# Kernel optimization log

Hardware: AMD Instinct MI355X
Metric: run time of the kernel (lower is better)

Reference implementation:

```python
import jax, jax.numpy as jnp
import numpy as np

B, N, CIN, COUT, K, L, NNZ = 4, 4096, 128, 128, 10, 50, 65536


def _spmm(idx, vals, X):
    # COO spmm: out[r] += vals * X[c]; idx: [2, nnz], X: [N, F]
    rows, cols = idx[0], idx[1]
    return jax.ops.segment_sum(vals[:, None] * X[cols], rows, num_segments=N)

_bspmm = jax.vmap(_spmm, in_axes=(0, 0, 0))  # batched over leading dim


def _hgnn_layer(phi_idx, phi_val, inv_idx, inv_val, fea, W, d):
    # original: ((phi @ diag(d)) @ phi_inv) @ (fea @ W)
    # identical math, evaluated right-to-left to stay sparse-dense only
    filt = jnp.einsum('bnc,co->bno', fea, W)            # [B,N,COUT]
    y = _bspmm(inv_idx, inv_val, filt)                  # phi_inv @ X
    y = d[None, :, None] * y                            # diag(d) @ .
    return _bspmm(phi_idx, phi_val, y)                  # phi @ .


def setup_inputs() -> dict:
    key = jax.random.key(0)
    ks = jax.random.split(key, 20)

    def coo(ki, kv):
        idx = jax.random.randint(ki, (B, 2, NNZ), 0, N, dtype=jnp.int32)
        val = jax.random.normal(kv, (B, NNZ), jnp.float32) * 0.05
        return idx, val

    phi1_idx, phi1_val = coo(ks[0], ks[1])
    phi1_inv_idx, phi1_inv_val = coo(ks[2], ks[3])
    phi2_idx, phi2_val = coo(ks[4], ks[5])
    phi2_inv_idx, phi2_inv_val = coo(ks[6], ks[7])
    fea = jax.random.normal(ks[8], (B, N, CIN), jnp.float32)
    joblst = jax.random.randint(ks[9], (B, L), 0, N, dtype=jnp.int64)

    xavier = float(np.sqrt(6.0 / (CIN + COUT)))
    W1 = jax.random.uniform(ks[10], (CIN, COUT), jnp.float32, -xavier, xavier)
    W2 = jax.random.uniform(ks[11], (CIN, COUT), jnp.float32, -xavier, xavier)
    d1 = jax.random.uniform(ks[12], (N,), jnp.float32, 0.9, 1.1)
    d2 = jax.random.uniform(ks[13], (N,), jnp.float32, 0.9, 1.1)
    s = float(1.0 / np.sqrt(N))
    W_ih = jax.random.uniform(ks[14], (N, COUT), jnp.float32, -s, s)
    W_hh = jax.random.uniform(ks[15], (N, N), jnp.float32, -s, s)
    b_ih = jax.random.uniform(ks[16], (N,), jnp.float32, -s, s)
    b_hh = jnp.zeros((N,), jnp.float32)
    sd = float(1.0 / np.sqrt(COUT))
    dense_W = jax.random.uniform(ks[17], (K, COUT), jnp.float32, -sd, sd)
    dense_b = jnp.zeros((K,), jnp.float32)
    item_emb = jax.random.normal(ks[18], (N, COUT), jnp.float32) * 0.01

    return dict(phi1_idx=phi1_idx, phi1_val=phi1_val, phi1_inv_idx=phi1_inv_idx,
                phi1_inv_val=phi1_inv_val, phi2_idx=phi2_idx, phi2_val=phi2_val,
                phi2_inv_idx=phi2_inv_idx, phi2_inv_val=phi2_inv_val,
                fea=fea, joblst=joblst, W1=W1, d1=d1, W2=W2, d2=d2,
                W_ih=W_ih, W_hh=W_hh, b_ih=b_ih, b_hh=b_hh,
                dense_W=dense_W, dense_b=dense_b, item_emb=item_emb)


def reference(phi1_idx, phi1_val, phi1_inv_idx, phi1_inv_val,
              phi2_idx, phi2_val, phi2_inv_idx, phi2_inv_val,
              fea, joblst, W1, d1, W2, d2, W_ih, W_hh, b_ih, b_hh,
              dense_W, dense_b, item_emb):
    # two hypergraph conv layers, summed
    out1 = _hgnn_layer(phi1_idx, phi1_val, phi1_inv_idx, phi1_inv_val, fea, W1, d1)
    out2 = _hgnn_layer(phi2_idx, phi2_val, phi2_inv_idx, phi2_inv_val, fea, W2, d2)
    res = out1 + out2                                   # [B,N,COUT]

    # RNN over job history embeddings (all joblst entries valid -> no -1 filter)
    xs = jnp.swapaxes(item_emb[joblst], 0, 1)           # [L,B,COUT]
    h0 = jnp.zeros((fea.shape[0], N), fea.dtype)

    def step(h, x):
        h = jnp.tanh(x @ W_ih.T + h @ W_hh.T + b_ih + b_hh)
        return h, None

    Emb, _ = jax.lax.scan(step, h0, xs)                 # last hidden: [B,N]

    res2 = jax.nn.gelu(jnp.einsum('bno,ko->bnk', res, dense_W) + dense_b,
                       approximate=False)               # [B,N,K]
    # (res3 * Emb2).permute back == res2 * gelu(Emb) broadcast over K
    return jax.nn.sigmoid(res2 * jax.nn.gelu(Emb, approximate=False)[:, :, None])
```

## Files before the change

kernel.cpp:

```cpp
#include <hip/hip_runtime.h>
#include <cstdint>
#include <cstddef>

#define NN   4096
#define LLC  50

__device__ __forceinline__ float bf2f(unsigned short u) {
    return __uint_as_float(((unsigned)u) << 16);
}
__device__ __forceinline__ unsigned short f2bf(float x) {
    unsigned b = __float_as_uint(x);
    return (unsigned short)((b + 0x7fffu + ((b >> 16) & 1u)) >> 16);
}

#if __has_builtin(__builtin_amdgcn_sdot4)
#define SDOT4(a, b, c) __builtin_amdgcn_sdot4((int)(a), (int)(b), (c), false)
#else
__device__ __forceinline__ int sdot4_sw(unsigned a, unsigned b, int c) {
    c += (int)(signed char)(a) * (int)(signed char)(b);
    c += (int)(signed char)(a >> 8) * (int)(signed char)(b >> 8);
    c += (int)(signed char)(a >> 16) * (int)(signed char)(b >> 16);
    c += (int)(signed char)(a >> 24) * (int)(signed char)(b >> 24);
    return c;
}
#define SDOT4(a, b, c) sdot4_sw((a), (b), (c))
#endif

#define DPPADD(v, ctrl, rmask) \
    ((v) + __builtin_amdgcn_update_dpp(0, (v), (ctrl), (rmask), 0xf, true))
__device__ __forceinline__ int wred64(int v) {
    v = DPPADD(v, 0x111, 0xf);
    v = DPPADD(v, 0x112, 0xf);
    v = DPPADD(v, 0x114, 0xf);
    v = DPPADD(v, 0x118, 0xf);
    v = DPPADD(v, 0x142, 0xa);
    v = DPPADD(v, 0x143, 0xc);
    return v;
}

__global__ __launch_bounds__(256) void k_w8(const float* __restrict__ W,
                                            uint4* __restrict__ out) {
    unsigned T = blockIdx.x * 256 + threadIdx.x;
    unsigned row = T >> 8, rem = T & 255;
    unsigned k4 = rem >> 6, lane = rem & 63;
    unsigned k0 = lane * 16 + k4 * 4;
    const float* src = W + ((size_t)row * 1024 + k0) * 4;
    unsigned q[4];
#pragma unroll
    for (int i = 0; i < 4; ++i) {
        float4 w = *(const float4*)(src + i * 4);
        int q0 = (int)rintf(fminf(fmaxf(w.x * 8192.f, -127.f), 127.f));
        int q1 = (int)rintf(fminf(fmaxf(w.y * 8192.f, -127.f), 127.f));
        int q2 = (int)rintf(fminf(fmaxf(w.z * 8192.f, -127.f), 127.f));
        int q3 = (int)rintf(fminf(fmaxf(w.w * 8192.f, -127.f), 127.f));
        q[i] = (q0 & 0xff) | ((q1 & 0xff) << 8) | ((q2 & 0xff) << 16) | ((q3 & 0xff) << 24);
    }
    out[(size_t)row * 256 + k4 * 64 + lane] = make_uint4(q[0], q[1], q[2], q[3]);
}

__global__ __launch_bounds__(128) void k_filt(const float* __restrict__ fea,
                                              const float* __restrict__ W1,
                                              const float* __restrict__ W2,
                                              unsigned short* __restrict__ f1,
                                              unsigned short* __restrict__ f2) {
    __shared__ float sfea[16][128];
    int t = threadIdx.x;
    int rb = blockIdx.x * 16;
    for (int r = 0; r < 16; ++r) sfea[r][t] = fea[(size_t)(rb + r) * 128 + t];
    __syncthreads();
    float a1[16], a2[16];
#pragma unroll
    for (int r = 0; r < 16; ++r) { a1[r] = 0.f; a2[r] = 0.f; }
    for (int c = 0; c < 128; c += 4) {
        float w10 = W1[(c + 0) * 128 + t], w11 = W1[(c + 1) * 128 + t];
        float w12 = W1[(c + 2) * 128 + t], w13 = W1[(c + 3) * 128 + t];
        float w20 = W2[(c + 0) * 128 + t], w21 = W2[(c + 1) * 128 + t];
        float w22 = W2[(c + 2) * 128 + t], w23 = W2[(c + 3) * 128 + t];
#pragma unroll
        for (int r = 0; r < 16; ++r) {
            float4 f = *(const float4*)&sfea[r][c];
            a1[r] += f.x * w10 + f.y * w11 + f.z * w12 + f.w * w13;
            a2[r] += f.x * w20 + f.y * w21 + f.z * w22 + f.w * w23;
        }
    }
#pragma unroll
    for (int r = 0; r < 16; ++r) {
        f1[(size_t)(rb + r) * 128 + t] = f2bf(a1[r]);
        f2[(size_t)(rb + r) * 128 + t] = f2bf(a2[r]);
    }
}

__global__ __launch_bounds__(256) void k_hist(const int* __restrict__ i0, const int* __restrict__ i1,
                                              const int* __restrict__ i2, const int* __restrict__ i3,
                                              int* __restrict__ counts) {
    __shared__ int lc[4096];
    int t = threadIdx.x;
#pragma unroll
    for (int i = 0; i < 16; ++i) lc[t + i * 256] = 0;
    __syncthreads();
    unsigned blk = blockIdx.x;
    unsigned s = blk >> 4, ch = blk & 15;
    unsigned m = s >> 2, b = s & 3;
    const int* ip = (m == 0) ? i0 : (m == 1) ? i1 : (m == 2) ? i2 : i3;
    unsigned base = b * 131072u + ch * 4096u;
#pragma unroll
    for (int i = 0; i < 16; ++i) {
        int r = ip[base + t + i * 256];
        atomicAdd(&lc[r], 1);
    }
    __syncthreads();
    int* cs = counts + s * 4096;
#pragma unroll
    for (int i = 0; i < 16; ++i) {
        int v = lc[t + i * 256];
        if (v) atomicAdd(cs + t + i * 256, v);
    }
}

__global__ __launch_bounds__(256) void k_scan(const int* __restrict__ counts,
                                              int* __restrict__ rowptr,
                                              int* __restrict__ cursor) {
    int s = blockIdx.x, t = threadIdx.x;
    int loc[16];
    int base = t * 16;
    const int* cs = counts + s * 4096;
    int run = 0;
#pragma unroll
    for (int i = 0; i < 16; ++i) { loc[i] = run; run += cs[base + i]; }
    int total = run;
    int lane = t & 63, wv = t >> 6;
    int v = total;
#pragma unroll
    for (int d = 1; d < 64; d <<= 1) { int u = __shfl_up(v, d, 64); if (lane >= d) v += u; }
    __shared__ int wt[4];
    if (lane == 63) wt[wv] = v;
    __syncthreads();
    int pre = v - total;
    for (int i = 0; i < wv; ++i) pre += wt[i];
    int* rp = rowptr + s * 4097;
    int* cu = cursor + s * 4096;
#pragma unroll
    for (int i = 0; i < 16; ++i) { rp[base + i] = pre + loc[i]; cu[base + i] = pre + loc[i]; }
    if (t == 255) rp[4096] = pre + total;
}

__global__ __launch_bounds__(256) void k_scatter(const int* __restrict__ i0, const int* __restrict__ i1,
                                                 const int* __restrict__ i2, const int* __restrict__ i3,
                                                 const float* __restrict__ v0, const float* __restrict__ v1,
                                                 const float* __restrict__ v2, const float* __restrict__ v3,
                                                 const float* __restrict__ d1, const float* __restrict__ d2,
                                                 int* __restrict__ cursor,
                                                 unsigned* __restrict__ ep) {
    unsigned gid = blockIdx.x * 256 + threadIdx.x;
    unsigned s = gid >> 16, e = gid & 65535;
    unsigned m = s >> 2, b = s & 3;
    const int* ip = (m == 0) ? i0 : (m == 1) ? i1 : (m == 2) ? i2 : i3;
    const float* vp = (m == 0) ? v0 : (m == 1) ? v1 : (m == 2) ? v2 : v3;
    int r = ip[(size_t)b * 131072 + e];
    int c = ip[(size_t)b * 131072 + 65536 + e];
    float v = vp[(size_t)b * 65536 + e];
    if (m == 1) v *= d1[c];
    if (m == 3) v *= d2[c];
    int pos = atomicAdd(cursor + s * 4096 + r, 1);
    ep[(size_t)s * 65536 + pos] = ((unsigned)c << 16) | (unsigned)f2bf(v);
}

__global__ __launch_bounds__(128) void k_gather1(const int* __restrict__ rowptr,
                                                 const unsigned* __restrict__ ep,
                                                 const unsigned short* __restrict__ filt1,
                                                 const unsigned short* __restrict__ filt2,
                                                 unsigned short* __restrict__ y1,
                                                 unsigned short* __restrict__ y2) {
    unsigned blk = blockIdx.x;
    unsigned b = blk & 3, row = (blk >> 2) & 4095, mm = blk >> 14;
    int s = (mm ? 8 : 0) + (int)b;
    const unsigned short* X = mm ? filt2 : filt1;
    unsigned short* Y = mm ? y2 : y1;
    int f = threadIdx.x;
    const int* rp = rowptr + s * 4097;
    int e0 = rp[row], e1 = rp[row + 1];
    float acc = 0.f;
    for (int e = e0; e < e1; ++e) {
        unsigned p = ep[(size_t)s * 65536 + e];
        float v = bf2f((unsigned short)(p & 0xffffu));
        int c = (int)(p >> 16);
        acc += v * bf2f(X[((size_t)b * 4096 + c) * 128 + f]);
    }
    Y[((size_t)b * 4096 + row) * 128 + f] = f2bf(acc);
}

__global__ __launch_bounds__(128) void k_gather2(const int* __restrict__ rowptr,
                                                 const unsigned* __restrict__ ep,
                                                 const unsigned short* __restrict__ y1,
                                                 const unsigned short* __restrict__ y2,
                                                 float* __restrict__ res) {
    unsigned blk = blockIdx.x;
    unsigned b = blk & 3, row = blk >> 2;
    int f = threadIdx.x;
    float acc = 0.f;
    {
        int s = 4 + (int)b;
        const int* rp = rowptr + s * 4097;
        int e0 = rp[row], e1 = rp[row + 1];
        for (int e = e0; e < e1; ++e) {
            unsigned p = ep[(size_t)s * 65536 + e];
            float v = bf2f((unsigned short)(p & 0xffffu));
            int c = (int)(p >> 16);
            acc += v * bf2f(y1[((size_t)b * 4096 + c) * 128 + f]);
        }
    }
    {
        int s = 12 + (int)b;
        const int* rp = rowptr + s * 4097;
        int e0 = rp[row], e1 = rp[row + 1];
        for (int e = e0; e < e1; ++e) {
            unsigned p = ep[(size_t)s * 65536 + e];
            float v = bf2f((unsigned short)(p & 0xffffu));
            int c = (int)(p >> 16);
            acc += v * bf2f(y2[((size_t)b * 4096 + c) * 128 + f]);
        }
    }
    res[((size_t)b * 4096 + row) * 128 + f] = acc;
}

__global__ __launch_bounds__(256) void k_xproj(const float* __restrict__ item_emb,
                                               const int* __restrict__ joblst,
                                               const float* __restrict__ W_ih,
                                               const float* __restrict__ b_ih,
                                               const float* __restrict__ b_hh,
                                               float* __restrict__ xp) {
    __shared__ float sx[8][128];
    int t = threadIdx.x;
    int n = blockIdx.x * 256 + t;
    int p0 = blockIdx.y * 8;
#pragma unroll
    for (int i = 0; i < 4; ++i) {
        int e2 = t + i * 256;
        int rr = e2 >> 7, c = e2 & 127;
        int p = p0 + rr;
        int b = p & 3, l = p >> 2;
        int j = joblst[b * LLC + l];
        sx[rr][c] = item_emb[(size_t)j * 128 + c];
    }
    __syncthreads();
    float acc[8];
#pragma unroll
    for (int r = 0; r < 8; ++r) acc[r] = 0.f;
    const float* wn = W_ih + (size_t)n * 128;
    for (int c = 0; c < 128; c += 4) {
        float4 w = *(const float4*)(wn + c);
#pragma unroll
        for (int r = 0; r < 8; ++r) {
            float4 xr = *(const float4*)&sx[r][c];
            acc[r] += xr.x * w.x + xr.y * w.y + xr.z * w.z + xr.w * w.w;
        }
    }
    float bias = b_ih[n] + b_hh[n];
#pragma unroll
    for (int r = 0; r < 8; ++r) xp[(size_t)(p0 + r) * NN + n] = acc[r] + bias;
}

__global__ __launch_bounds__(256) void k_rnn_first(const float* __restrict__ xp,
                                                   unsigned* __restrict__ hq0) {
    unsigned D = blockIdx.x * 256 + threadIdx.x;
    unsigned b = D >> 10, rowd = D & 1023;
    unsigned d = 0;
#pragma unroll
    for (int i = 0; i < 4; ++i) {
        float h = tanhf(xp[(size_t)b * NN + rowd * 4 + i]);
        int q = (int)rintf(h * 127.f);
        d |= ((unsigned)(q & 0xff)) << (8 * i);
    }
    hq0[D] = d;
}

__global__ __launch_bounds__(256) void k_rnn_step(const uint4* __restrict__ Wp,
                                                  const float* __restrict__ xp,
                                                  const unsigned* __restrict__ hin,
                                                  unsigned* __restrict__ hout,
                                                  float* __restrict__ hfin, int l) {
    __shared__ int red[4][16];
    __shared__ unsigned char hpk[4][4][4];
    int t = threadIdx.x;
    int lane = t & 63, wv = t >> 6;
    int blk = blockIdx.x;
    int row_base = ((blk & 7) * 32 + (blk >> 3)) * 16;
    int wrow = row_base + wv * 4;

    uint4 H[4][4];
#pragma unroll
    for (int b = 0; b < 4; ++b)
#pragma unroll
        for (int k4 = 0; k4 < 4; ++k4)
            H[b][k4] = *(const uint4*)(hin + (size_t)b * 1024 + lane * 16 + k4 * 4);

    uint4 W[4][4];
#pragma unroll
    for (int r = 0; r < 4; ++r)
#pragma unroll
        for (int k4 = 0; k4 < 4; ++k4)
            W[r][k4] = Wp[(size_t)(wrow + r) * 256 + k4 * 64 + lane];

    int acc[4][4];
#pragma unroll
    for (int r = 0; r < 4; ++r)
#pragma unroll
        for (int b = 0; b < 4; ++b) acc[r][b] = 0;

#pragma unroll
    for (int k4 = 0; k4 < 4; ++k4)
#pragma unroll
        for (int r = 0; r < 4; ++r)
#pragma unroll
            for (int b = 0; b < 4; ++b) {
                acc[r][b] = SDOT4(W[r][k4].x, H[b][k4].x, acc[r][b]);
                acc[r][b] = SDOT4(W[r][k4].y, H[b][k4].y, acc[r][b]);
                acc[r][b] = SDOT4(W[r][k4].z, H[b][k4].z, acc[r][b]);
                acc[r][b] = SDOT4(W[r][k4].w, H[b][k4].w, acc[r][b]);
            }

#pragma unroll
    for (int r = 0; r < 4; ++r)
#pragma unroll
        for (int b = 0; b < 4; ++b) acc[r][b] = wred64(acc[r][b]);
    if (lane == 63) {
#pragma unroll
        for (int b = 0; b < 4; ++b) {
            int4 q = { acc[0][b], acc[1][b], acc[2][b], acc[3][b] };
            *(int4*)&red[wv][b * 4] = q;
        }
    }
    if (lane < 16) {
        const float SC = 1.f / (8192.f * 127.f);
        int b = lane >> 2, rr = lane & 3;
        int row = wrow + rr;
        float pre = (float)red[wv][lane] * SC + xp[(size_t)(l * 4 + b) * NN + row];
        float hnew = tanhf(pre);
        if (l == LLC - 1) hfin[(size_t)b * NN + row] = hnew;
        int q = (int)rintf(hnew * 127.f);
        hpk[wv][b][rr] = (unsigned char)(q & 0xff);
    }
    if (lane < 4) {
        unsigned d = *(const unsigned*)&hpk[wv][lane][0];
        hout[(size_t)lane * 1024 + (row_base >> 2) + wv] = d;
    }
}

__global__ __launch_bounds__(256) void k_final(const float* __restrict__ res,
                                               const float* __restrict__ dW,
                                               const float* __restrict__ db,
                                               const float* __restrict__ hfin,
                                               float* __restrict__ out) {
    __shared__ float4 sres4[512];
    __shared__ float sdw[10 * 132];
    int t = threadIdx.x;
    int row0 = blockIdx.x * 16;
    {
        const float4* src = (const float4*)(res + (size_t)row0 * 128);
        sres4[t] = src[t];
        sres4[t + 256] = src[t + 256];
    }
    for (int i = t; i < 1280; i += 256) { int k = i >> 7, c = i & 127; sdw[k * 132 + c] = dW[i]; }
    __syncthreads();
    int r = t >> 4, k = t & 15;
    if (k < 10) {
        const float* rr = (const float*)sres4 + r * 128;
        const float* wk = sdw + k * 132;
        float acc = 0.f;
#pragma unroll
        for (int c = 0; c < 128; c += 4) {
            float4 a = *(const float4*)(rr + c);
            float4 w = *(const float4*)(wk + c);
            acc += a.x * w.x + a.y * w.y + a.z * w.z + a.w * w.w;
        }
        float pre = acc + db[k];
        int grow = row0 + r;
        int b = grow >> 12, n = grow & 4095;
        float e = hfin[(size_t)b * NN + n];
        float g1 = 0.5f * pre * (1.f + erff(pre * 0.70710678118f));
        float ge = 0.5f * e * (1.f + erff(e * 0.70710678118f));
        out[(size_t)grow * 10 + k] = 1.f / (1.f + __expf(-g1 * ge));
    }
}

extern "C" void kernel_launch(void* const* d_in, const int* in_sizes, int n_in,
                              void* d_out, int out_size, void* d_ws, size_t ws_size,
                              hipStream_t stream) {
    const int*   phi1_idx = (const int*)d_in[0];
    const float* phi1_val = (const float*)d_in[1];
    const int*   inv1_idx = (const int*)d_in[2];
    const float* inv1_val = (const float*)d_in[3];
    const int*   phi2_idx = (const int*)d_in[4];
    const float* phi2_val = (const float*)d_in[5];
    const int*   inv2_idx = (const int*)d_in[6];
    const float* inv2_val = (const float*)d_in[7];
    const float* fea      = (const float*)d_in[8];
    const int*   joblst   = (const int*)d_in[9];
    const float* W1       = (const float*)d_in[10];
    const float* d1       = (const float*)d_in[11];
    const float* W2       = (const float*)d_in[12];
    const float* d2       = (const float*)d_in[13];
    const float* W_ih     = (const float*)d_in[14];
    const float* W_hh     = (const float*)d_in[15];
    const float* b_ih     = (const float*)d_in[16];
    const float* b_hh     = (const float*)d_in[17];
    const float* dense_W  = (const float*)d_in[18];
    const float* dense_b  = (const float*)d_in[19];
    const float* item_emb = (const float*)d_in[20];

    float* ws = (float*)d_ws;
    unsigned short* filt1 = (unsigned short*)ws;
    unsigned short* filt2 = (unsigned short*)(ws + 1048576);
    unsigned short* y1    = (unsigned short*)(ws + 2097152);
    unsigned short* y2    = (unsigned short*)(ws + 3145728);
    float* res  = ws + 4194304;
    float* xp   = ws + 6291456;
    float* hfin = ws + 7110656;
    unsigned* hq  = (unsigned*)(ws + 7127040);
    uint4* w8p = (uint4*)(ws + 7135232);
    int*   counts = (int*)(ws + 11329536);
    int*   rowptr = (int*)(ws + 11395072);
    int*   cursor = (int*)(ws + 11460624);
    unsigned* ep  = (unsigned*)(ws + 11526160);

    hipMemsetAsync(counts, 0, 16 * 4096 * sizeof(int), stream);

    k_w8<<<4096, 256, 0, stream>>>(W_hh, w8p);
    k_filt<<<1024, 128, 0, stream>>>(fea, W1, W2, filt1, filt2);
    k_xproj<<<dim3(16, 25), 256, 0, stream>>>(item_emb, joblst, W_ih, b_ih, b_hh, xp);

    k_hist<<<256, 256, 0, stream>>>(inv1_idx, phi1_idx, inv2_idx, phi2_idx, counts);
    k_scan<<<16, 256, 0, stream>>>(counts, rowptr, cursor);
    k_scatter<<<4096, 256, 0, stream>>>(inv1_idx, phi1_idx, inv2_idx, phi2_idx,
                                        inv1_val, phi1_val, inv2_val, phi2_val,
                                        d1, d2, cursor, ep);

    k_gather1<<<32768, 128, 0, stream>>>(rowptr, ep, filt1, filt2, y1, y2);
    k_gather2<<<16384, 128, 0, stream>>>(rowptr, ep, y1, y2, res);

    k_rnn_first<<<16, 256, 0, stream>>>(xp, hq);
    for (int l = 1; l < LLC; ++l) {
        const unsigned* hin = hq + (size_t)((l - 1) & 1) * 4096;
        unsigned*       hout = hq + (size_t)(l & 1) * 4096;
        k_rnn_step<<<256, 256, 0, stream>>>(w8p, xp, hin, hout, hfin, l);
    }
    k_final<<<1024, 256, 0, stream>>>(res, dense_W, dense_b, hfin, (float*)d_out);
}
```

Measured before the change: 551.8 us.

## Fuse RNN time steps into one persistent cooperative kernel with grid barrier

```diff
diff --git a/kernel.cpp b/kernel.cpp
--- a/kernel.cpp
+++ b/kernel.cpp
@@ -1,4 +1,5 @@
 #include <hip/hip_runtime.h>
+#include <hip/hip_cooperative_groups.h>
 #include <cstdint>
 #include <cstddef>
 
@@ -99,7 +100,9 @@
     for (int i = 0; i < 16; ++i) lc[t + i * 256] = 0;
     __syncthreads();
     unsigned blk = blockIdx.x;
-    unsigned s = blk >> 4, ch = blk & 15;
+    unsigned p = blk & 7, j = blk >> 3;
+    unsigned s = (j < 16) ? p : p + 8;
+    unsigned ch = j & 15;
     unsigned m = s >> 2, b = s & 3;
     const int* ip = (m == 0) ? i0 : (m == 1) ? i1 : (m == 2) ? i2 : i3;
     unsigned base = b * 131072u + ch * 4096u;
@@ -151,8 +154,10 @@
                                                  const float* __restrict__ d1, const float* __restrict__ d2,
                                                  int* __restrict__ cursor,
                                                  unsigned* __restrict__ ep) {
-    unsigned gid = blockIdx.x * 256 + threadIdx.x;
-    unsigned s = gid >> 16, e = gid & 65535;
+    unsigned blk = blockIdx.x;
+    unsigned p = blk & 7, j = blk >> 3;
+    unsigned s = (j < 256) ? p : p + 8;
+    unsigned e = ((j & 255) << 8) | threadIdx.x;
     unsigned m = s >> 2, b = s & 3;
     const int* ip = (m == 0) ? i0 : (m == 1) ? i1 : (m == 2) ? i2 : i3;
     const float* vp = (m == 0) ? v0 : (m == 1) ? v1 : (m == 2) ? v2 : v3;
@@ -181,9 +186,9 @@
     int e0 = rp[row], e1 = rp[row + 1];
     float acc = 0.f;
     for (int e = e0; e < e1; ++e) {
-        unsigned p = ep[(size_t)s * 65536 + e];
-        float v = bf2f((unsigned short)(p & 0xffffu));
-        int c = (int)(p >> 16);
+        unsigned pp = ep[(size_t)s * 65536 + e];
+        float v = bf2f((unsigned short)(pp & 0xffffu));
+        int c = (int)(pp >> 16);
         acc += v * bf2f(X[((size_t)b * 4096 + c) * 128 + f]);
     }
     Y[((size_t)b * 4096 + row) * 128 + f] = f2bf(acc);
@@ -203,9 +208,9 @@
         const int* rp = rowptr + s * 4097;
         int e0 = rp[row], e1 = rp[row + 1];
         for (int e = e0; e < e1; ++e) {
-            unsigned p = ep[(size_t)s * 65536 + e];
-            float v = bf2f((unsigned short)(p & 0xffffu));
-            int c = (int)(p >> 16);
+            unsigned pp = ep[(size_t)s * 65536 + e];
+            float v = bf2f((unsigned short)(pp & 0xffffu));
+            int c = (int)(pp >> 16);
             acc += v * bf2f(y1[((size_t)b * 4096 + c) * 128 + f]);
         }
     }
@@ -214,9 +219,9 @@
         const int* rp = rowptr + s * 4097;
         int e0 = rp[row], e1 = rp[row + 1];
         for (int e = e0; e < e1; ++e) {
-            unsigned p = ep[(size_t)s * 65536 + e];
-            float v = bf2f((unsigned short)(p & 0xffffu));
-            int c = (int)(p >> 16);
+            unsigned pp = ep[(size_t)s * 65536 + e];
+            float v = bf2f((unsigned short)(pp & 0xffffu));
+            int c = (int)(pp >> 16);
             acc += v * bf2f(y2[((size_t)b * 4096 + c) * 128 + f]);
         }
     }
@@ -260,25 +265,11 @@
     for (int r = 0; r < 8; ++r) xp[(size_t)(p0 + r) * NN + n] = acc[r] + bias;
 }
 
-__global__ __launch_bounds__(256) void k_rnn_first(const float* __restrict__ xp,
-                                                   unsigned* __restrict__ hq0) {
-    unsigned D = blockIdx.x * 256 + threadIdx.x;
-    unsigned b = D >> 10, rowd = D & 1023;
-    unsigned d = 0;
-#pragma unroll
-    for (int i = 0; i < 4; ++i) {
-        float h = tanhf(xp[(size_t)b * NN + rowd * 4 + i]);
-        int q = (int)rintf(h * 127.f);
-        d |= ((unsigned)(q & 0xff)) << (8 * i);
-    }
-    hq0[D] = d;
-}
-
-__global__ __launch_bounds__(256) void k_rnn_step(const uint4* __restrict__ Wp,
-                                                  const float* __restrict__ xp,
-                                                  const unsigned* __restrict__ hin,
-                                                  unsigned* __restrict__ hout,
-                                                  float* __restrict__ hfin, int l) {
+__global__ __launch_bounds__(256) void k_rnn_all(const uint4* __restrict__ Wp,
+                                                 const float* __restrict__ xp,
+                                                 unsigned* __restrict__ hq,
+                                                 float* __restrict__ hfin,
+                                                 int* __restrict__ bar) {
     __shared__ int red[4][16];
     __shared__ unsigned char hpk[4][4][4];
     int t = threadIdx.x;
@@ -287,13 +278,6 @@
     int row_base = ((blk & 7) * 32 + (blk >> 3)) * 16;
     int wrow = row_base + wv * 4;
 
-    uint4 H[4][4];
-#pragma unroll
-    for (int b = 0; b < 4; ++b)
-#pragma unroll
-        for (int k4 = 0; k4 < 4; ++k4)
-            H[b][k4] = *(const uint4*)(hin + (size_t)b * 1024 + lane * 16 + k4 * 4);
-
     uint4 W[4][4];
 #pragma unroll
     for (int r = 0; r < 4; ++r)
@@ -301,48 +285,69 @@
         for (int k4 = 0; k4 < 4; ++k4)
             W[r][k4] = Wp[(size_t)(wrow + r) * 256 + k4 * 64 + lane];
 
-    int acc[4][4];
-#pragma unroll
-    for (int r = 0; r < 4; ++r)
-#pragma unroll
-        for (int b = 0; b < 4; ++b) acc[r][b] = 0;
-
-#pragma unroll
-    for (int k4 = 0; k4 < 4; ++k4)
-#pragma unroll
-        for (int r = 0; r < 4; ++r)
-#pragma unroll
-            for (int b = 0; b < 4; ++b) {
-                acc[r][b] = SDOT4(W[r][k4].x, H[b][k4].x, acc[r][b]);
-                acc[r][b] = SDOT4(W[r][k4].y, H[b][k4].y, acc[r][b]);
-                acc[r][b] = SDOT4(W[r][k4].z, H[b][k4].z, acc[r][b]);
-                acc[r][b] = SDOT4(W[r][k4].w, H[b][k4].w, acc[r][b]);
+    const float SC = 1.f / (8192.f * 127.f);
+
+    for (int l = 0; l < LLC; ++l) {
+        if (l > 0) {
+            const unsigned* hin = hq + (size_t)((l - 1) & 1) * 4096;
+            uint4 H[4][4];
+#pragma unroll
+            for (int b = 0; b < 4; ++b)
+#pragma unroll
+                for (int k4 = 0; k4 < 4; ++k4)
+                    H[b][k4] = *(const uint4*)(hin + (size_t)b * 1024 + lane * 16 + k4 * 4);
+            int acc[4][4];
+#pragma unroll
+            for (int r = 0; r < 4; ++r)
+#pragma unroll
+                for (int b = 0; b < 4; ++b) acc[r][b] = 0;
+#pragma unroll
+            for (int k4 = 0; k4 < 4; ++k4)
+#pragma unroll
+                for (int r = 0; r < 4; ++r)
+#pragma unroll
+                    for (int b = 0; b < 4; ++b) {
+                        acc[r][b] = SDOT4(W[r][k4].x, H[b][k4].x, acc[r][b]);
+                        acc[r][b] = SDOT4(W[r][k4].y, H[b][k4].y, acc[r][b]);
+                        acc[r][b] = SDOT4(W[r][k4].z, H[b][k4].z, acc[r][b]);
+                        acc[r][b] = SDOT4(W[r][k4].w, H[b][k4].w, acc[r][b]);
+                    }
+#pragma unroll
+            for (int r = 0; r < 4; ++r)
+#pragma unroll
+                for (int b = 0; b < 4; ++b) acc[r][b] = wred64(acc[r][b]);
+            if (lane == 63) {
+#pragma unroll
+                for (int b = 0; b < 4; ++b) {
+                    int4 q = { acc[0][b], acc[1][b], acc[2][b], acc[3][b] };
+                    *(int4*)&red[wv][b * 4] = q;
+                }
             }
-
-#pragma unroll
-    for (int r = 0; r < 4; ++r)
-#pragma unroll
-        for (int b = 0; b < 4; ++b) acc[r][b] = wred64(acc[r][b]);
-    if (lane == 63) {
-#pragma unroll
-        for (int b = 0; b < 4; ++b) {
-            int4 q = { acc[0][b], acc[1][b], acc[2][b], acc[3][b] };
-            *(int4*)&red[wv][b * 4] = q;
-        }
-    }
-    if (lane < 16) {
-        const float SC = 1.f / (8192.f * 127.f);
-        int b = lane >> 2, rr = lane & 3;
-        int row = wrow + rr;
-        float pre = (float)red[wv][lane] * SC + xp[(size_t)(l * 4 + b) * NN + row];
-        float hnew = tanhf(pre);
-        if (l == LLC - 1) hfin[(size_t)b * NN + row] = hnew;
-        int q = (int)rintf(hnew * 127.f);
-        hpk[wv][b][rr] = (unsigned char)(q & 0xff);
-    }
-    if (lane < 4) {
-        unsigned d = *(const unsigned*)&hpk[wv][lane][0];
-        hout[(size_t)lane * 1024 + (row_base >> 2) + wv] = d;
+        }
+        if (lane < 16) {
+            int b = lane >> 2, rr = lane & 3;
+            int row = wrow + rr;
+            float a = (l > 0) ? (float)red[wv][lane] * SC : 0.f;
+            float pre = a + xp[(size_t)(l * 4 + b) * NN + row];
+            float hnew = tanhf(pre);
+            if (l == LLC - 1) hfin[(size_t)b * NN + row] = hnew;
+            int q = (int)rintf(hnew * 127.f);
+            hpk[wv][b][rr] = (unsigned char)(q & 0xff);
+        }
+        if (lane < 4) {
+            unsigned d = *(const unsigned*)&hpk[wv][lane][0];
+            hq[(size_t)(l & 1) * 4096 + (size_t)lane * 1024 + (row_base >> 2) + wv] = d;
+        }
+        __syncthreads();
+        if (t == 0) {
+            __threadfence();
+            atomicAdd(bar, 1);
+            int target = 256 * (l + 1);
+            while (__hip_atomic_load(bar, __ATOMIC_RELAXED, __HIP_MEMORY_SCOPE_AGENT) < target)
+                __builtin_amdgcn_s_sleep(1);
+            __threadfence();
+        }
+        __syncthreads();
     }
 }
 
@@ -422,8 +427,10 @@
     int*   rowptr = (int*)(ws + 11395072);
     int*   cursor = (int*)(ws + 11460624);
     unsigned* ep  = (unsigned*)(ws + 11526160);
+    int*   bar    = (int*)(ws + 12574736);
 
     hipMemsetAsync(counts, 0, 16 * 4096 * sizeof(int), stream);
+    hipMemsetAsync(bar, 0, sizeof(int), stream);
 
     k_w8<<<4096, 256, 0, stream>>>(W_hh, w8p);
     k_filt<<<1024, 128, 0, stream>>>(fea, W1, W2, filt1, filt2);
@@ -438,11 +445,11 @@
     k_gather1<<<32768, 128, 0, stream>>>(rowptr, ep, filt1, filt2, y1, y2);
     k_gather2<<<16384, 128, 0, stream>>>(rowptr, ep, y1, y2, res);
 
-    k_rnn_first<<<16, 256, 0, stream>>>(xp, hq);
-    for (int l = 1; l < LLC; ++l) {
-        const unsigned* hin = hq + (size_t)((l - 1) & 1) * 4096;
-        unsigned*       hout = hq + (size_t)(l & 1) * 4096;
-        k_rnn_step<<<256, 256, 0, stream>>>(w8p, xp, hin, hout, hfin, l);
-    }
+    {
+        void* args[] = { (void*)&w8p, (void*)&xp, (void*)&hq, (void*)&hfin, (void*)&bar };
+        hipLaunchCooperativeKernel((const void*)k_rnn_all, dim3(256), dim3(256),
+                                   args, 0, stream);
+    }
+
     k_final<<<1024, 256, 0, stream>>>(res, dense_W, dense_b, hfin, (float*)d_out);
 }
```

Result: slower. 1.418 ms (+157.0%).
